# Kernel tuning notes

Hardware: AMD Instinct MI355X
Metric: run time of the kernel (lower is better)

Reference implementation:

```python
import jax, jax.numpy as jnp
import numpy as np

NUM_HEADS = 16
HIDDEN = 1024
HEAD = HIDDEN // NUM_HEADS
NEG_INF = -10000.0


def setup_inputs() -> dict:
    key = jax.random.key(0)
    k1, k2, k3, k4 = jax.random.split(key, 4)
    B, S = 4, 2048
    x = jax.random.normal(k1, (B, S, HIDDEN), dtype=jnp.float32)
    pos_embeds = jax.random.normal(k2, (S, HIDDEN), dtype=jnp.float32)
    # Dense(3*hidden, use_bias=False) and Dense(hidden, use_bias=False)
    Wqkv = jax.random.normal(k3, (HIDDEN, 3 * HIDDEN), dtype=jnp.float32) / np.sqrt(HIDDEN)
    Wo = jax.random.normal(k4, (HIDDEN, HIDDEN), dtype=jnp.float32) / np.sqrt(HIDDEN)
    return {"x": x, "pos_embeds": pos_embeds, "Wqkv": Wqkv, "Wo": Wo}


def _compute_qkv(t, Wqkv):
    # rearrange '... s (k n h) -> k ... n s h', k=3, n=NUM_HEADS
    proj = t @ Wqkv  # [..., s, 3*n*h]
    proj = proj.reshape(*t.shape[:-1], 3, NUM_HEADS, HEAD)  # [..., s, 3, n, h]
    # move: k first, then leading dims, then n, s, h
    nd = proj.ndim
    perm = (nd - 3,) + tuple(range(nd - 4)) + (nd - 2, nd - 4, nd - 1)
    return jnp.transpose(proj, perm)  # [3, ..., n, s, h]


def reference(x, pos_embeds, Wqkv, Wo):
    S = x.shape[-2]
    q, k, v = _compute_qkv(x, Wqkv)  # each [B, n, S, h]
    pos_qkv = _compute_qkv(pos_embeds[:S], Wqkv)  # [3, n, S, h]
    pos_q, pos_k = pos_qkv[0], pos_qkv[1]
    q = q + pos_q  # broadcast over batch
    k = k + pos_k
    scores = jnp.einsum('bnqh,bnkh->bnqk', q, k) / np.sqrt(HEAD).astype(np.float32)
    causal = jnp.arange(S)[:, None] < jnp.arange(S)[None, :]  # strict upper triangle (future)
    scores = jnp.where(causal, NEG_INF, scores)
    probs = jax.nn.softmax(scores, axis=-1)
    # dropout deterministic (training=False) -> identity
    combined = jnp.einsum('bnqk,bnkh->bnqh', probs, v)  # [B, n, S, h]
    combined = jnp.transpose(combined, (0, 2, 1, 3)).reshape(x.shape[0], S, HIDDEN)  # '... n q h -> ... q (n h)'
    out = combined @ Wo
    return out
```

## Files before the change

### kernel.cpp

```cpp
#include <hip/hip_runtime.h>


typedef float f32x4 __attribute__((ext_vector_type(4)));
typedef short bf16x8 __attribute__((ext_vector_type(8)));
typedef short bf16x4 __attribute__((ext_vector_type(4)));

#define MFMA_BF16(a, b, c) __builtin_amdgcn_mfma_f32_16x16x32_bf16((a), (b), (c), 0, 0, 0)

#if __has_builtin(__builtin_amdgcn_mfma_f32_16x16x16bf16_1k)
#define HAVE_MFMA16 1
#define MFMA_BF16_K16(a, b, c) __builtin_amdgcn_mfma_f32_16x16x16bf16_1k((a), (b), (c), 0, 0, 0)
#else
#define HAVE_MFMA16 0
#endif

__device__ __forceinline__ short f2bf(float f) {
  union { float f; unsigned u; } v; v.f = f;
  unsigned u = v.u;
  u += 0x7fffu + ((u >> 16) & 1u);
  return (short)(u >> 16);
}

__device__ __forceinline__ float bf2f(short s) {
  union { unsigned u; float f; } v;
  v.u = ((unsigned)(unsigned short)s) << 16;
  return v.f;
}

__device__ __forceinline__ int pack_bf2_fast(float a, float b) {
  union { float f; unsigned u; } va, vb; va.f = a; vb.f = b;
  unsigned ua = va.u + 0x8000u;
  unsigned ub = vb.u + 0x8000u;
  return (int)((ua >> 16) | (ub & 0xffff0000u));
}

__device__ const int QT_X[30] = {5,6,7,8,9,10,11,11,12,12,13,13,14,14,15,15,
                                 4,10, 3,9,15, 2,8,14, 1,7,13, 0,6,12};
__device__ const int CH_X[30] = {0,0,0,0,0,0,0,1,0,1,0,1,0,1,0,1,
                                 0,1, 0,1,2, 0,1,2, 0,1,2, 0,1,2};
__device__ const int START_QT[16] = {0,1,2,3,4,5,6,8,10,12,14,16,18,21,24,27};

__global__ __launch_bounds__(256) void prep_x(const float* __restrict__ x,
                                              const float* __restrict__ pos,
                                              short* __restrict__ xb,
                                              short* __restrict__ xpb) {
  int i = blockIdx.x * 256 + threadIdx.x;
  int idx = i * 4;
  const float4 xv = *(const float4*)(x + idx);
  const float4 pv = *(const float4*)(pos + (idx & ((2048 * 1024) - 1)));
  short4 a, b;
  a.x = f2bf(xv.x); a.y = f2bf(xv.y); a.z = f2bf(xv.z); a.w = f2bf(xv.w);
  b.x = f2bf(xv.x + pv.x); b.y = f2bf(xv.y + pv.y);
  b.z = f2bf(xv.z + pv.z); b.w = f2bf(xv.w + pv.w);
  *(short4*)(xb + idx) = a;
  *(short4*)(xpb + idx) = b;
}

__global__ __launch_bounds__(256) void transpose_w(const float* __restrict__ in,
                                                   short* __restrict__ out,
                                                   int K, int N) {
  __shared__ float tile[32][33];
  int n0 = blockIdx.x * 32, k0 = blockIdx.y * 32;
  int c = threadIdx.x & 31, r0 = threadIdx.x >> 5;
  for (int i = 0; i < 4; i++) {
    int r = r0 + i * 8;
    tile[r][c] = in[(size_t)(k0 + r) * N + n0 + c];
  }
  __syncthreads();
  for (int i = 0; i < 4; i++) {
    int r = r0 + i * 8;
    out[(size_t)(n0 + r) * K + k0 + c] = f2bf(tile[c][r]);
  }
}

__global__ __launch_bounds__(256) void gemm_qkv(const short* __restrict__ xb,
                                                const short* __restrict__ xpb,
                                                const short* __restrict__ wt,
                                                short* __restrict__ qg,
                                                short* __restrict__ kg,
                                                short* __restrict__ vtg) {
  __shared__ __align__(16) short As[128 * 72];
  __shared__ __align__(16) short Bs[128 * 72];
  const int bm = blockIdx.x, bn = blockIdx.y;
  const short* __restrict__ A = (bn < 16) ? xpb : xb;
  const int tid = threadIdx.x;
  const int lane = tid & 63, wid = tid >> 6;
  const int wm = wid & 1, wn = wid >> 1;
  const int quad = lane >> 4, l16 = lane & 15;
  const f32x4 fzero = {0.f, 0.f, 0.f, 0.f};
  f32x4 acc[4][4];
  for (int mt = 0; mt < 4; mt++)
    for (int nt = 0; nt < 4; nt++) acc[mt][nt] = fzero;
  const int arow0 = bm * 128, brow0 = bn * 128;
  for (int k0 = 0; k0 < 1024; k0 += 64) {
    for (int i = 0; i < 4; i++) {
      int cc = tid + i * 256;
      int r = cc >> 3, kc = cc & 7;
      *(int4*)(As + r * 72 + kc * 8) =
          *(const int4*)(A + (size_t)(arow0 + r) * 1024 + k0 + kc * 8);
      *(int4*)(Bs + r * 72 + kc * 8) =
          *(const int4*)(wt + (size_t)(brow0 + r) * 1024 + k0 + kc * 8);
    }
    __syncthreads();
    for (int ks = 0; ks < 2; ks++) {
      bf16x8 af[4], bfr[4];
      for (int mt = 0; mt < 4; mt++)
        af[mt] = *(const bf16x8*)(As + (wm * 64 + mt * 16 + l16) * 72 + ks * 32 + quad * 8);
      for (int nt = 0; nt < 4; nt++)
        bfr[nt] = *(const bf16x8*)(Bs + (wn * 64 + nt * 16 + l16) * 72 + ks * 32 + quad * 8);
      for (int mt = 0; mt < 4; mt++)
        for (int nt = 0; nt < 4; nt++)
          acc[mt][nt] = MFMA_BF16(af[mt], bfr[nt], acc[mt][nt]);
    }
    __syncthreads();
  }
  for (int nt = 0; nt < 4; nt++) {
    int col = bn * 128 + wn * 64 + nt * 16 + l16;
    int kk = col >> 10, head = (col >> 6) & 15, hh = col & 63;
    for (int mt = 0; mt < 4; mt++) {
      int rowb = bm * 128 + wm * 64 + mt * 16 + quad * 4;
      int b = rowb >> 11, s0 = rowb & 2047;
      if (kk == 2) {
        short4 sv;
        sv.x = f2bf(acc[mt][nt][0]); sv.y = f2bf(acc[mt][nt][1]);
        sv.z = f2bf(acc[mt][nt][2]); sv.w = f2bf(acc[mt][nt][3]);
        *(short4*)(vtg + (size_t)((b * 16 + head) * 64 + hh) * 2048 + s0) = sv;
      } else {
        short* __restrict__ dst = (kk == 0) ? qg : kg;
        float scale = (kk == 0) ? 0.18033688f : 1.0f;
        for (int r = 0; r < 4; r++)
          dst[(size_t)((b * 16 + head) * 2048 + s0 + r) * 64 + hh] =
              f2bf(acc[mt][nt][r] * scale);
      }
    }
  }
}

__global__ __launch_bounds__(256, 3) void attn_part(const short* __restrict__ qg,
                                                    const short* __restrict__ kg,
                                                    const short* __restrict__ vtg,
                                                    short* __restrict__ pO,
                                                    float* __restrict__ pL) {
  const int xi = blockIdx.x;
  const int qt = QT_X[xi], ch = CH_X[xi];
  const int head = blockIdx.y, b = blockIdx.z;
  const int bh = b * 16 + head;
  const int p = bh * 30 + START_QT[qt] + ch;
  const short* __restrict__ Q = qg + (size_t)bh * 2048 * 64;
  const short* __restrict__ K = kg + (size_t)bh * 2048 * 64;
  const short* __restrict__ VT = vtg + (size_t)bh * 64 * 2048;
  __shared__ __align__(16) short Ks[2][64 * 72];
  __shared__ __align__(16) short Vs[2][64 * 72];
#if !HAVE_MFMA16
  __shared__ __align__(16) short Ps[4][16 * 72];
#endif
  const int tid = threadIdx.x, lane = tid & 63, w = tid >> 6;
  const int quad = lane >> 4, l16 = lane & 15;
  const f32x4 fzero = {0.f, 0.f, 0.f, 0.f};

  bf16x8 bq[2][2];
#pragma unroll
  for (int sub = 0; sub < 2; sub++) {
    int qrow = qt * 128 + w * 32 + sub * 16 + l16;
#pragma unroll
    for (int ks = 0; ks < 2; ks++)
      bq[sub][ks] = *(const bf16x8*)(Q + (size_t)qrow * 64 + ks * 32 + quad * 8);
  }
  f32x4 acco[2][4];
  f32x4 lrun[2];
#pragma unroll
  for (int sub = 0; sub < 2; sub++) {
    for (int nt = 0; nt < 4; nt++) acco[sub][nt] = fzero;
    lrun[sub] = fzero;
  }

  const int kt0 = ch * 12;
  const int kt1 = min(kt0 + 12, 2 * qt + 2);
  const int qmin_w = qt * 128 + w * 32;

  const int sr0 = tid >> 3, sc0 = (tid & 7) * 8;
  const int sr1 = (tid + 256) >> 3, sc1 = sc0;

  int4 kreg[2], vreg[2];
  {
    int kv0 = kt0 * 64;
    kreg[0] = *(const int4*)(K + (size_t)(kv0 + sr0) * 64 + sc0);
    kreg[1] = *(const int4*)(K + (size_t)(kv0 + sr1) * 64 + sc1);
    vreg[0] = *(const int4*)(VT + (size_t)sr0 * 2048 + kv0 + sc0);
    vreg[1] = *(const int4*)(VT + (size_t)sr1 * 2048 + kv0 + sc1);
    *(int4*)(&Ks[0][sr0 * 72 + sc0]) = kreg[0];
    *(int4*)(&Ks[0][sr1 * 72 + sc1]) = kreg[1];
    *(int4*)(&Vs[0][sr0 * 72 + sc0]) = vreg[0];
    *(int4*)(&Vs[0][sr1 * 72 + sc1]) = vreg[1];
  }
  __syncthreads();

  for (int kt = kt0; kt < kt1; kt++) {
    const int cur = (kt - kt0) & 1;
    if (kt + 1 < kt1) {
      int kv0 = (kt + 1) * 64;
      kreg[0] = *(const int4*)(K + (size_t)(kv0 + sr0) * 64 + sc0);
      kreg[1] = *(const int4*)(K + (size_t)(kv0 + sr1) * 64 + sc1);
      vreg[0] = *(const int4*)(VT + (size_t)sr0 * 2048 + kv0 + sc0);
      vreg[1] = *(const int4*)(VT + (size_t)sr1 * 2048 + kv0 + sc1);
    }

    if (kt * 64 <= qmin_w + 31) {
      f32x4 accs[2][4];
#pragma unroll
      for (int sub = 0; sub < 2; sub++)
        for (int nt = 0; nt < 4; nt++) accs[sub][nt] = fzero;
#pragma unroll
      for (int ks = 0; ks < 2; ks++)
#pragma unroll
        for (int nt = 0; nt < 4; nt++) {
          bf16x8 ak = *(const bf16x8*)(&Ks[cur][(nt * 16 + l16) * 72 + ks * 32 + quad * 8]);
          accs[0][nt] = MFMA_BF16(ak, bq[0][ks], accs[0][nt]);
          accs[1][nt] = MFMA_BF16(ak, bq[1][ks], accs[1][nt]);
        }

      if ((kt + 1) * 64 > qmin_w) {
#pragma unroll
        for (int sub = 0; sub < 2; sub++) {
          int q = qmin_w + sub * 16 + l16;
#pragma unroll
          for (int nt = 0; nt < 4; nt++) {
            int kv = kt * 64 + nt * 16 + quad * 4;
#pragma unroll
            for (int r = 0; r < 4; r++)
              if (kv + r > q) accs[sub][nt][r] = -1e30f;
          }
        }
      }

#pragma unroll
      for (int sub = 0; sub < 2; sub++)
#pragma unroll
        for (int nt = 0; nt < 4; nt++) {
#pragma unroll
          for (int r = 0; r < 4; r++) accs[sub][nt][r] = exp2f(accs[sub][nt][r]);
          lrun[sub] += accs[sub][nt];
        }

#if HAVE_MFMA16
#pragma unroll
      for (int kk = 0; kk < 4; kk++) {
        union { int2 i2; bf16x4 v; } p0, p1;
        p0.i2.x = pack_bf2_fast(accs[0][kk][0], accs[0][kk][1]);
        p0.i2.y = pack_bf2_fast(accs[0][kk][2], accs[0][kk][3]);
        p1.i2.x = pack_bf2_fast(accs[1][kk][0], accs[1][kk][1]);
        p1.i2.y = pack_bf2_fast(accs[1][kk][2], accs[1][kk][3]);
#pragma unroll
        for (int nth = 0; nth < 4; nth++) {
          bf16x4 av = *(const bf16x4*)(&Vs[cur][(nth * 16 + l16) * 72 + kk * 16 + quad * 4]);
          acco[0][nth] = MFMA_BF16_K16(av, p0.v, acco[0][nth]);
          acco[1][nth] = MFMA_BF16_K16(av, p1.v, acco[1][nth]);
        }
      }
#else
      short* P = Ps[w];
#pragma unroll
      for (int sub = 0; sub < 2; sub++) {
#pragma unroll
        for (int nt = 0; nt < 4; nt++) {
          int2 pk;
          pk.x = pack_bf2_fast(accs[sub][nt][0], accs[sub][nt][1]);
          pk.y = pack_bf2_fast(accs[sub][nt][2], accs[sub][nt][3]);
          *(int2*)(P + l16 * 72 + nt * 16 + quad * 4) = pk;
        }
#pragma unroll
        for (int ks2 = 0; ks2 < 2; ks2++) {
          bf16x8 bp = *(const bf16x8*)(P + l16 * 72 + ks2 * 32 + quad * 8);
#pragma unroll
          for (int nth = 0; nth < 4; nth++) {
            bf16x8 av = *(const bf16x8*)(&Vs[cur][(nth * 16 + l16) * 72 + ks2 * 32 + quad * 8]);
            acco[sub][nth] = MFMA_BF16(av, bp, acco[sub][nth]);
          }
        }
      }
#endif
    }

    if (kt + 1 < kt1) {
      const int nxt = cur ^ 1;
      *(int4*)(&Ks[nxt][sr0 * 72 + sc0]) = kreg[0];
      *(int4*)(&Ks[nxt][sr1 * 72 + sc1]) = kreg[1];
      *(int4*)(&Vs[nxt][sr0 * 72 + sc0]) = vreg[0];
      *(int4*)(&Vs[nxt][sr1 * 72 + sc1]) = vreg[1];
    }
    __syncthreads();
  }

#pragma unroll
  for (int sub = 0; sub < 2; sub++) {
    float lh = (lrun[sub][0] + lrun[sub][1]) + (lrun[sub][2] + lrun[sub][3]);
    lh += __shfl_xor(lh, 16);
    lh += __shfl_xor(lh, 32);
    int qloc = w * 32 + sub * 16 + l16;
    if (quad == 0) pL[p * 128 + qloc] = lh;
    size_t base = (size_t)p * 8192 + (size_t)qloc * 64;
#pragma unroll
    for (int nth = 0; nth < 4; nth++) {
      short4 sv;
      sv.x = f2bf(acco[sub][nth][0]);
      sv.y = f2bf(acco[sub][nth][1]);
      sv.z = f2bf(acco[sub][nth][2]);
      sv.w = f2bf(acco[sub][nth][3]);
      *(short4*)(pO + base + nth * 16 + quad * 4) = sv;
    }
  }
}

__global__ __launch_bounds__(256) void attn_merge(const short* __restrict__ pO,
                                                  const float* __restrict__ pL,
                                                  short* __restrict__ comb) {
  const int qt = blockIdx.x, head = blockIdx.y, b = blockIdx.z;
  const int bh = b * 16 + head;
  const int nch = (2 * qt + 13) / 12;
  const int p0 = bh * 30 + START_QT[qt];
  const int t = threadIdx.x;
  const int qloc = t >> 1, hh = (t & 1) * 32;

  float l = 0.f;
  for (int c = 0; c < nch; c++) l += pL[(p0 + c) * 128 + qloc];
  const float inv = 1.f / l;

  float acc[32];
#pragma unroll
  for (int j = 0; j < 32; j++) acc[j] = 0.f;
  for (int c = 0; c < nch; c++) {
    const short* src = pO + (size_t)(p0 + c) * 8192 + (size_t)qloc * 64 + hh;
#pragma unroll
    for (int v = 0; v < 4; v++) {
      short4 d0 = *(const short4*)(src + v * 8);
      short4 d1 = *(const short4*)(src + v * 8 + 4);
      acc[v * 8 + 0] += bf2f(d0.x); acc[v * 8 + 1] += bf2f(d0.y);
      acc[v * 8 + 2] += bf2f(d0.z); acc[v * 8 + 3] += bf2f(d0.w);
      acc[v * 8 + 4] += bf2f(d1.x); acc[v * 8 + 5] += bf2f(d1.y);
      acc[v * 8 + 6] += bf2f(d1.z); acc[v * 8 + 7] += bf2f(d1.w);
    }
  }
  size_t base = (size_t)(b * 2048 + qt * 128 + qloc) * 1024 + head * 64 + hh;
#pragma unroll
  for (int v = 0; v < 8; v++) {
    short4 sv;
    sv.x = f2bf(acc[v * 4 + 0] * inv);
    sv.y = f2bf(acc[v * 4 + 1] * inv);
    sv.z = f2bf(acc[v * 4 + 2] * inv);
    sv.w = f2bf(acc[v * 4 + 3] * inv);
    *(short4*)(comb + base + v * 4) = sv;
  }
}

__global__ __launch_bounds__(256) void gemm_out(const short* __restrict__ A,
                                                const short* __restrict__ wt,
                                                float* __restrict__ out) {
  __shared__ __align__(16) short As[128 * 72];
  __shared__ __align__(16) short Bs[128 * 72];
  const int bm = blockIdx.x, bn = blockIdx.y;
  const int tid = threadIdx.x;
  const int lane = tid & 63, wid = tid >> 6;
  const int wm = wid & 1, wn = wid >> 1;
  const int quad = lane >> 4, l16 = lane & 15;
  const f32x4 fzero = {0.f, 0.f, 0.f, 0.f};
  f32x4 acc[4][4];
  for (int mt = 0; mt < 4; mt++)
    for (int nt = 0; nt < 4; nt++) acc[mt][nt] = fzero;
  const int arow0 = bm * 128, brow0 = bn * 128;
  for (int k0 = 0; k0 < 1024; k0 += 64) {
    for (int i = 0; i < 4; i++) {
      int cc = tid + i * 256;
      int r = cc >> 3, kc = cc & 7;
      *(int4*)(As + r * 72 + kc * 8) =
          *(const int4*)(A + (size_t)(arow0 + r) * 1024 + k0 + kc * 8);
      *(int4*)(Bs + r * 72 + kc * 8) =
          *(const int4*)(wt + (size_t)(brow0 + r) * 1024 + k0 + kc * 8);
    }
    __syncthreads();
    for (int ks = 0; ks < 2; ks++) {
      bf16x8 af[4], bfr[4];
      for (int mt = 0; mt < 4; mt++)
        af[mt] = *(const bf16x8*)(As + (wm * 64 + mt * 16 + l16) * 72 + ks * 32 + quad * 8);
      for (int nt = 0; nt < 4; nt++)
        bfr[nt] = *(const bf16x8*)(Bs + (wn * 64 + nt * 16 + l16) * 72 + ks * 32 + quad * 8);
      for (int mt = 0; mt < 4; mt++)
        for (int nt = 0; nt < 4; nt++)
          acc[mt][nt] = MFMA_BF16(af[mt], bfr[nt], acc[mt][nt]);
    }
    __syncthreads();
  }
  for (int nt = 0; nt < 4; nt++) {
    int col = bn * 128 + wn * 64 + nt * 16 + l16;
    for (int mt = 0; mt < 4; mt++) {
      int rowb = bm * 128 + wm * 64 + mt * 16 + quad * 4;
      for (int r = 0; r < 4; r++)
        out[(size_t)(rowb + r) * 1024 + col] = acc[mt][nt][r];
    }
  }
}

extern "C" void kernel_launch(void* const* d_in, const int* in_sizes, int n_in,
                              void* d_out, int out_size, void* d_ws, size_t ws_size,
                              hipStream_t stream) {
  const float* x    = (const float*)d_in[0];
  const float* pos  = (const float*)d_in[1];
  const float* Wqkv = (const float*)d_in[2];
  const float* Wo   = (const float*)d_in[3];
  float* out = (float*)d_out;

  char* ws = (char*)d_ws;
  const size_t SZ = (size_t)8192 * 1024 * 2;
  short* xb    = (short*)(ws);
  short* xpb   = (short*)(ws + SZ);
  short* pO    = (short*)(ws);
  float* pL    = (float*)(ws + (size_t)1920 * 8192 * 2);
  short* q     = (short*)(ws + 2 * SZ);
  short* k     = (short*)(ws + 3 * SZ);
  short* vt    = (short*)(ws + 4 * SZ);
  short* comb  = (short*)(ws + 5 * SZ);
  short* wqkvt = (short*)(ws + 6 * SZ);
  short* wot   = (short*)(ws + 6 * SZ + (size_t)3072 * 1024 * 2);

  prep_x<<<8192, 256, 0, stream>>>(x, pos, xb, xpb);
  transpose_w<<<dim3(96, 32), 256, 0, stream>>>(Wqkv, wqkvt, 1024, 3072);
  transpose_w<<<dim3(32, 32), 256, 0, stream>>>(Wo, wot, 1024, 1024);
  gemm_qkv<<<dim3(64, 24), 256, 0, stream>>>(xb, xpb, wqkvt, q, k, vt);
  attn_part<<<dim3(30, 16, 4), 256, 0, stream>>>(q, k, vt, pO, pL);
  attn_merge<<<dim3(16, 16, 4), 256, 0, stream>>>(pO, pL, comb);
  gemm_out<<<dim3(64, 8), 256, 0, stream>>>(comb, wot, out);
}
```

Baseline: 327.3 us.

## Swizzle attention LDS tiles, remap grids for XCD locality, use hardware bf16 packing

Replaces the padded K/V shared-memory tiles in attention with XOR/rotation swizzled layouts to avoid bank conflicts and reduce LDS footprint. It also adds s_setprio around MFMA sections and replaces the software bf16 pack with v_cvt_pk_bf16_f32. The partial output is staged through LDS so global stores are coalesced. All four main kernels switch to 1D grids whose block index is remapped so that consecutive blocks on the same XCD share data for L2 locality. These changes alter rounding slightly (RNE vs round-half-up) and add a sync at the attention epilogue.

```diff
diff --git a/kernel.cpp b/kernel.cpp
--- a/kernel.cpp
+++ b/kernel.cpp
@@ -27,11 +27,17 @@
   return v.f;
 }
 
-__device__ __forceinline__ int pack_bf2_fast(float a, float b) {
-  union { float f; unsigned u; } va, vb; va.f = a; vb.f = b;
-  unsigned ua = va.u + 0x8000u;
-  unsigned ub = vb.u + 0x8000u;
-  return (int)((ua >> 16) | (ub & 0xffff0000u));
+__device__ __forceinline__ int cvt_pk_bf16(float lo, float hi) {
+  int r;
+  asm("v_cvt_pk_bf16_f32 %0, %1, %2" : "=v"(r) : "v"(lo), "v"(hi));
+  return r;
+}
+
+__device__ __forceinline__ int swzK(int row, int colbyte) {
+  return row * 64 + (((colbyte) ^ ((row & 7) << 4)) >> 1);
+}
+__device__ __forceinline__ int swzV(int row, int colbyte) {
+  return row * 64 + ((((colbyte >> 3) + row) & 15) << 2);
 }
 
 __device__ const int QT_X[30] = {5,6,7,8,9,10,11,11,12,12,13,13,14,14,15,15,
@@ -81,7 +87,10 @@
                                                 short* __restrict__ vtg) {
   __shared__ __align__(16) short As[128 * 72];
   __shared__ __align__(16) short Bs[128 * 72];
-  const int bm = blockIdx.x, bn = blockIdx.y;
+  const int n = blockIdx.x;
+  const int idx = n >> 3;
+  const int bm = (n & 7) * 8 + (idx & 7);
+  const int bn = idx >> 3;
   const short* __restrict__ A = (bn < 16) ? xpb : xb;
   const int tid = threadIdx.x;
   const int lane = tid & 63, wid = tid >> 6;
@@ -141,16 +150,17 @@
                                                     const short* __restrict__ vtg,
                                                     short* __restrict__ pO,
                                                     float* __restrict__ pL) {
-  const int xi = blockIdx.x;
-  const int qt = QT_X[xi], ch = CH_X[xi];
-  const int head = blockIdx.y, b = blockIdx.z;
-  const int bh = b * 16 + head;
+  const int n = blockIdx.x;
+  const int i = n >> 3;
+  const int bh = (n & 7) * 8 + i / 30;
+  const int slot = i % 30;
+  const int qt = QT_X[slot], ch = CH_X[slot];
   const int p = bh * 30 + START_QT[qt] + ch;
   const short* __restrict__ Q = qg + (size_t)bh * 2048 * 64;
   const short* __restrict__ K = kg + (size_t)bh * 2048 * 64;
   const short* __restrict__ VT = vtg + (size_t)bh * 64 * 2048;
-  __shared__ __align__(16) short Ks[2][64 * 72];
-  __shared__ __align__(16) short Vs[2][64 * 72];
+  __shared__ __align__(16) short Ks[2][64 * 64];
+  __shared__ __align__(16) short Vs[2][64 * 64];
 #if !HAVE_MFMA16
   __shared__ __align__(16) short Ps[4][16 * 72];
 #endif
@@ -178,20 +188,26 @@
   const int kt1 = min(kt0 + 12, 2 * qt + 2);
   const int qmin_w = qt * 128 + w * 32;
 
-  const int sr0 = tid >> 3, sc0 = (tid & 7) * 8;
-  const int sr1 = (tid + 256) >> 3, sc1 = sc0;
+  const int sr0 = tid >> 3, sr1 = sr0 + 32;
+  const int scs = (tid & 7) * 8;
+  const int scb = (tid & 7) * 16;
+  const int oK0 = swzK(sr0, scb), oK1 = swzK(sr1, scb);
+  const int oV0a = swzV(sr0, scb), oV0b = swzV(sr0, scb + 8);
+  const int oV1a = swzV(sr1, scb), oV1b = swzV(sr1, scb + 8);
 
   int4 kreg[2], vreg[2];
   {
     int kv0 = kt0 * 64;
-    kreg[0] = *(const int4*)(K + (size_t)(kv0 + sr0) * 64 + sc0);
-    kreg[1] = *(const int4*)(K + (size_t)(kv0 + sr1) * 64 + sc1);
-    vreg[0] = *(const int4*)(VT + (size_t)sr0 * 2048 + kv0 + sc0);
-    vreg[1] = *(const int4*)(VT + (size_t)sr1 * 2048 + kv0 + sc1);
-    *(int4*)(&Ks[0][sr0 * 72 + sc0]) = kreg[0];
-    *(int4*)(&Ks[0][sr1 * 72 + sc1]) = kreg[1];
-    *(int4*)(&Vs[0][sr0 * 72 + sc0]) = vreg[0];
-    *(int4*)(&Vs[0][sr1 * 72 + sc1]) = vreg[1];
+    kreg[0] = *(const int4*)(K + (size_t)(kv0 + sr0) * 64 + scs);
+    kreg[1] = *(const int4*)(K + (size_t)(kv0 + sr1) * 64 + scs);
+    vreg[0] = *(const int4*)(VT + (size_t)sr0 * 2048 + kv0 + scs);
+    vreg[1] = *(const int4*)(VT + (size_t)sr1 * 2048 + kv0 + scs);
+    *(int4*)(&Ks[0][oK0]) = kreg[0];
+    *(int4*)(&Ks[0][oK1]) = kreg[1];
+    *(int2*)(&Vs[0][oV0a]) = make_int2(vreg[0].x, vreg[0].y);
+    *(int2*)(&Vs[0][oV0b]) = make_int2(vreg[0].z, vreg[0].w);
+    *(int2*)(&Vs[0][oV1a]) = make_int2(vreg[1].x, vreg[1].y);
+    *(int2*)(&Vs[0][oV1b]) = make_int2(vreg[1].z, vreg[1].w);
   }
   __syncthreads();
 
@@ -199,10 +215,10 @@
     const int cur = (kt - kt0) & 1;
     if (kt + 1 < kt1) {
       int kv0 = (kt + 1) * 64;
-      kreg[0] = *(const int4*)(K + (size_t)(kv0 + sr0) * 64 + sc0);
-      kreg[1] = *(const int4*)(K + (size_t)(kv0 + sr1) * 64 + sc1);
-      vreg[0] = *(const int4*)(VT + (size_t)sr0 * 2048 + kv0 + sc0);
-      vreg[1] = *(const int4*)(VT + (size_t)sr1 * 2048 + kv0 + sc1);
+      kreg[0] = *(const int4*)(K + (size_t)(kv0 + sr0) * 64 + scs);
+      kreg[1] = *(const int4*)(K + (size_t)(kv0 + sr1) * 64 + scs);
+      vreg[0] = *(const int4*)(VT + (size_t)sr0 * 2048 + kv0 + scs);
+      vreg[1] = *(const int4*)(VT + (size_t)sr1 * 2048 + kv0 + scs);
     }
 
     if (kt * 64 <= qmin_w + 31) {
@@ -210,14 +226,16 @@
 #pragma unroll
       for (int sub = 0; sub < 2; sub++)
         for (int nt = 0; nt < 4; nt++) accs[sub][nt] = fzero;
+      __builtin_amdgcn_s_setprio(1);
 #pragma unroll
       for (int ks = 0; ks < 2; ks++)
 #pragma unroll
         for (int nt = 0; nt < 4; nt++) {
-          bf16x8 ak = *(const bf16x8*)(&Ks[cur][(nt * 16 + l16) * 72 + ks * 32 + quad * 8]);
+          bf16x8 ak = *(const bf16x8*)(&Ks[cur][swzK(nt * 16 + l16, ks * 64 + quad * 16)]);
           accs[0][nt] = MFMA_BF16(ak, bq[0][ks], accs[0][nt]);
           accs[1][nt] = MFMA_BF16(ak, bq[1][ks], accs[1][nt]);
         }
+      __builtin_amdgcn_s_setprio(0);
 
       if ((kt + 1) * 64 > qmin_w) {
 #pragma unroll
@@ -243,20 +261,22 @@
         }
 
 #if HAVE_MFMA16
+      __builtin_amdgcn_s_setprio(1);
 #pragma unroll
       for (int kk = 0; kk < 4; kk++) {
         union { int2 i2; bf16x4 v; } p0, p1;
-        p0.i2.x = pack_bf2_fast(accs[0][kk][0], accs[0][kk][1]);
-        p0.i2.y = pack_bf2_fast(accs[0][kk][2], accs[0][kk][3]);
-        p1.i2.x = pack_bf2_fast(accs[1][kk][0], accs[1][kk][1]);
-        p1.i2.y = pack_bf2_fast(accs[1][kk][2], accs[1][kk][3]);
+        p0.i2.x = cvt_pk_bf16(accs[0][kk][0], accs[0][kk][1]);
+        p0.i2.y = cvt_pk_bf16(accs[0][kk][2], accs[0][kk][3]);
+        p1.i2.x = cvt_pk_bf16(accs[1][kk][0], accs[1][kk][1]);
+        p1.i2.y = cvt_pk_bf16(accs[1][kk][2], accs[1][kk][3]);
 #pragma unroll
         for (int nth = 0; nth < 4; nth++) {
-          bf16x4 av = *(const bf16x4*)(&Vs[cur][(nth * 16 + l16) * 72 + kk * 16 + quad * 4]);
+          bf16x4 av = *(const bf16x4*)(&Vs[cur][swzV(nth * 16 + l16, kk * 32 + quad * 8)]);
           acco[0][nth] = MFMA_BF16_K16(av, p0.v, acco[0][nth]);
           acco[1][nth] = MFMA_BF16_K16(av, p1.v, acco[1][nth]);
         }
       }
+      __builtin_amdgcn_s_setprio(0);
 #else
       short* P = Ps[w];
 #pragma unroll
@@ -264,8 +284,8 @@
 #pragma unroll
         for (int nt = 0; nt < 4; nt++) {
           int2 pk;
-          pk.x = pack_bf2_fast(accs[sub][nt][0], accs[sub][nt][1]);
-          pk.y = pack_bf2_fast(accs[sub][nt][2], accs[sub][nt][3]);
+          pk.x = cvt_pk_bf16(accs[sub][nt][0], accs[sub][nt][1]);
+          pk.y = cvt_pk_bf16(accs[sub][nt][2], accs[sub][nt][3]);
           *(int2*)(P + l16 * 72 + nt * 16 + quad * 4) = pk;
         }
 #pragma unroll
@@ -273,7 +293,11 @@
           bf16x8 bp = *(const bf16x8*)(P + l16 * 72 + ks2 * 32 + quad * 8);
 #pragma unroll
           for (int nth = 0; nth < 4; nth++) {
-            bf16x8 av = *(const bf16x8*)(&Vs[cur][(nth * 16 + l16) * 72 + ks2 * 32 + quad * 8]);
+            int r = nth * 16 + l16;
+            int4 t4;
+            *(int2*)&t4.x = *(const int2*)(&Vs[cur][swzV(r, ks2 * 64 + quad * 16)]);
+            *(int2*)&t4.z = *(const int2*)(&Vs[cur][swzV(r, ks2 * 64 + quad * 16 + 8)]);
+            bf16x8 av = *(const bf16x8*)&t4;
             acco[sub][nth] = MFMA_BF16(av, bp, acco[sub][nth]);
           }
         }
@@ -283,10 +307,12 @@
 
     if (kt + 1 < kt1) {
       const int nxt = cur ^ 1;
-      *(int4*)(&Ks[nxt][sr0 * 72 + sc0]) = kreg[0];
-      *(int4*)(&Ks[nxt][sr1 * 72 + sc1]) = kreg[1];
-      *(int4*)(&Vs[nxt][sr0 * 72 + sc0]) = vreg[0];
-      *(int4*)(&Vs[nxt][sr1 * 72 + sc1]) = vreg[1];
+      *(int4*)(&Ks[nxt][oK0]) = kreg[0];
+      *(int4*)(&Ks[nxt][oK1]) = kreg[1];
+      *(int2*)(&Vs[nxt][oV0a]) = make_int2(vreg[0].x, vreg[0].y);
+      *(int2*)(&Vs[nxt][oV0b]) = make_int2(vreg[0].z, vreg[0].w);
+      *(int2*)(&Vs[nxt][oV1a]) = make_int2(vreg[1].x, vreg[1].y);
+      *(int2*)(&Vs[nxt][oV1b]) = make_int2(vreg[1].z, vreg[1].w);
     }
     __syncthreads();
   }
@@ -298,24 +324,41 @@
     lh += __shfl_xor(lh, 32);
     int qloc = w * 32 + sub * 16 + l16;
     if (quad == 0) pL[p * 128 + qloc] = lh;
-    size_t base = (size_t)p * 8192 + (size_t)qloc * 64;
+  }
+
+  short* Ob = &Ks[0][0];
+#pragma unroll
+  for (int sub = 0; sub < 2; sub++) {
+    int qloc = w * 32 + sub * 16 + l16;
 #pragma unroll
     for (int nth = 0; nth < 4; nth++) {
-      short4 sv;
-      sv.x = f2bf(acco[sub][nth][0]);
-      sv.y = f2bf(acco[sub][nth][1]);
-      sv.z = f2bf(acco[sub][nth][2]);
-      sv.w = f2bf(acco[sub][nth][3]);
-      *(short4*)(pO + base + nth * 16 + quad * 4) = sv;
-    }
+      int2 pk;
+      pk.x = cvt_pk_bf16(acco[sub][nth][0], acco[sub][nth][1]);
+      pk.y = cvt_pk_bf16(acco[sub][nth][2], acco[sub][nth][3]);
+      *(int2*)(Ob + swzK(qloc, nth * 32 + quad * 8)) = pk;
+    }
+  }
+  __syncthreads();
+  {
+    const int row = tid >> 1;
+    const int hb = (tid & 1) * 64;
+    int4 v0 = *(const int4*)(Ob + swzK(row, hb));
+    int4 v1 = *(const int4*)(Ob + swzK(row, hb + 16));
+    int4 v2 = *(const int4*)(Ob + swzK(row, hb + 32));
+    int4 v3 = *(const int4*)(Ob + swzK(row, hb + 48));
+    int4* dst = (int4*)(pO + (size_t)p * 8192 + tid * 32);
+    dst[0] = v0; dst[1] = v1; dst[2] = v2; dst[3] = v3;
   }
 }
 
 __global__ __launch_bounds__(256) void attn_merge(const short* __restrict__ pO,
                                                   const float* __restrict__ pL,
                                                   short* __restrict__ comb) {
-  const int qt = blockIdx.x, head = blockIdx.y, b = blockIdx.z;
-  const int bh = b * 16 + head;
+  const int n = blockIdx.x;
+  const int i = n >> 3;
+  const int bh = (n & 7) * 8 + (i >> 4);
+  const int qt = i & 15;
+  const int head = bh & 15, b = bh >> 4;
   const int nch = (2 * qt + 13) / 12;
   const int p0 = bh * 30 + START_QT[qt];
   const int t = threadIdx.x;
@@ -357,7 +400,10 @@
                                                 float* __restrict__ out) {
   __shared__ __align__(16) short As[128 * 72];
   __shared__ __align__(16) short Bs[128 * 72];
-  const int bm = blockIdx.x, bn = blockIdx.y;
+  const int n = blockIdx.x;
+  const int idx = n >> 3;
+  const int bm = (n & 7) * 8 + (idx & 7);
+  const int bn = idx >> 3;
   const int tid = threadIdx.x;
   const int lane = tid & 63, wid = tid >> 6;
   const int wm = wid & 1, wn = wid >> 1;
@@ -424,8 +470,8 @@
   prep_x<<<8192, 256, 0, stream>>>(x, pos, xb, xpb);
   transpose_w<<<dim3(96, 32), 256, 0, stream>>>(Wqkv, wqkvt, 1024, 3072);
   transpose_w<<<dim3(32, 32), 256, 0, stream>>>(Wo, wot, 1024, 1024);
-  gemm_qkv<<<dim3(64, 24), 256, 0, stream>>>(xb, xpb, wqkvt, q, k, vt);
-  attn_part<<<dim3(30, 16, 4), 256, 0, stream>>>(q, k, vt, pO, pL);
-  attn_merge<<<dim3(16, 16, 4), 256, 0, stream>>>(pO, pL, comb);
-  gemm_out<<<dim3(64, 8), 256, 0, stream>>>(comb, wot, out);
-}
+  gemm_qkv<<<dim3(1536), 256, 0, stream>>>(xb, xpb, wqkvt, q, k, vt);
+  attn_part<<<dim3(1920), 256, 0, stream>>>(q, k, vt, pO, pL);
+  attn_merge<<<dim3(1024), 256, 0, stream>>>(pO, pL, comb);
+  gemm_out<<<dim3(512), 256, 0, stream>>>(comb, wot, out);
+}
```

After: 293.7 us. 10.3% less time.
